# Performance work log

Hardware: AMD Instinct MI355X
Metric: run time of the kernel (lower is better)

The kernel has to match this reference:

```python
import jax, jax.numpy as jnp
import numpy as np

B, C, H, W = 32, 512, 32, 32


def setup_inputs() -> dict:
    key = jax.random.key(0)
    ks = jax.random.split(key, 7)
    c2 = C // 2
    s_in = (1.0 / C) ** 0.5   # torch Conv2d default init scale (kernel 1x1)
    s_c2 = (1.0 / c2) ** 0.5
    return {
        "x": jax.random.normal(ks[0], (B, C, H, W), jnp.float32),
        "Wk": jax.random.normal(ks[1], (c2, C), jnp.float32) * s_in,
        "bk": jax.random.normal(ks[2], (c2,), jnp.float32) * s_in,
        "Wv": jax.random.normal(ks[3], (c2, C), jnp.float32) * s_in,
        "bv": jax.random.normal(ks[4], (c2,), jnp.float32) * s_in,
        "Wo": jax.random.normal(ks[5], (C, c2), jnp.float32) * s_c2,
        "bo": jax.random.normal(ks[6], (C,), jnp.float32) * s_c2,
    }


def reference(x, Wk, bk, Wv, bv, Wo, bo):
    Bn, Cn, Hn, Wn = x.shape
    c2 = Cn // 2
    M = Hn * Wn
    # 1x1 convs as channel contractions
    k = jnp.einsum('oc,bchw->bohw', Wk, x) + bk[None, :, None, None]   # [B,c2,H,W]
    v = jnp.einsum('oc,bchw->bohw', Wv, x) + bv[None, :, None, None]   # [B,c2,H,W]
    # torch .reshape(B, M, c2) reinterprets memory (NOT a transpose) -> same in jnp
    v = v.reshape(Bn, M, c2)                                           # [B,M,c2]
    kf = k.reshape(Bn, c2, M)                                          # [B,c2,M]
    # cov_feature: k^T I_hat k with I_hat = (1/M)I - (1/M^2)11^T
    #            = (1/M) k^T k - (1/M^2) s s^T,  s = sum over channels
    gram = jnp.einsum('bcm,bcn->bmn', kf, kf) / M                      # [B,M,M]
    s = kf.sum(axis=1)                                                 # [B,M]
    cov = gram - (s[:, :, None] * s[:, None, :]) / (M * M)
    attn = jax.nn.softmax(cov * (c2 ** -0.5), axis=-1)                 # [B,M,M]
    out = jnp.einsum('bmn,bnc->bmc', attn, v)                          # [B,M,c2]
    # torch .view(B, c2, H, W) is also a raw memory reinterpretation
    out = out.reshape(Bn, c2, Hn, Wn)
    out = jnp.einsum('oc,bchw->bohw', Wo, out) + bo[None, :, None, None]
    return out + x
```

## Files before the change

### kernel.cpp

```cpp
#include <hip/hip_runtime.h>


typedef short bf8 __attribute__((ext_vector_type(8)));
typedef float f32x4 __attribute__((ext_vector_type(4)));

#define MFMA16(a, b, c) __builtin_amdgcn_mfma_f32_16x16x32_bf16((a), (b), (c), 0, 0, 0)

__device__ __forceinline__ short f2bf(float x) {
  unsigned u = __float_as_uint(x);
  u += 0x7fffu + ((u >> 16) & 1u);
  return (short)(u >> 16);
}

__device__ __forceinline__ void gll16(const short* g, void* l) {
  __builtin_amdgcn_global_load_lds(
      (const __attribute__((address_space(1))) unsigned int*)g,
      (__attribute__((address_space(3))) unsigned int*)l, 16, 0, 0);
}

__device__ __forceinline__ void gemm_core(const short* __restrict__ A,
                                          const short* __restrict__ B,
                                          int ldA, int ldB, int ksteps,
                                          char* smem, f32x4 acc[4][4]) {
  const int tid = threadIdx.x;
  const int w = tid >> 6, l = tid & 63;
  const int q = l >> 4, i = l & 15;
  const int wm = w & 1, wn = w >> 1;
  const int srow = l >> 3;
  const int gcol = ((l & 7) ^ srow) * 8;
  f32x4 zz = {0.f, 0.f, 0.f, 0.f};
  #pragma unroll
  for (int mt = 0; mt < 4; ++mt)
    #pragma unroll
    for (int nt = 0; nt < 4; ++nt) acc[mt][nt] = zz;

  for (int ks = 0; ks < ksteps; ++ks) {
    __syncthreads();
    const short* Ak = A + ks * 64 + gcol;
    const short* Bk = B + ks * 64 + gcol;
    #pragma unroll
    for (int j = 0; j < 4; ++j) {
      int s = w * 4 + j;
      size_t row = (size_t)(s * 8 + srow);
      gll16(Ak + row * ldA, smem + s * 1024);
      gll16(Bk + row * ldB, smem + 16384 + s * 1024);
    }
    __syncthreads();
    #pragma unroll
    for (int kq = 0; kq < 2; ++kq) {
      int sw = ((kq * 4 + q) ^ (i & 7)) * 16;
      bf8 af[4], bq[4];
      #pragma unroll
      for (int mt = 0; mt < 4; ++mt)
        af[mt] = *(const bf8*)(smem + (wm * 64 + mt * 16 + i) * 128 + sw);
      #pragma unroll
      for (int nt = 0; nt < 4; ++nt)
        bq[nt] = *(const bf8*)(smem + 16384 + (wn * 64 + nt * 16 + i) * 128 + sw);
      #pragma unroll
      for (int mt = 0; mt < 4; ++mt)
        #pragma unroll
        for (int nt = 0; nt < 4; ++nt)
          acc[mt][nt] = MFMA16(af[mt], bq[nt], acc[mt][nt]);
    }
  }
}

__global__ __launch_bounds__(256) void p0_xpose(const float* __restrict__ x,
                                                short* __restrict__ xT) {
  __shared__ float lds[64][65];
  int cb = blockIdx.x, sb = blockIdx.y, b = blockIdx.z;
  int t = threadIdx.x;
  int c0 = cb * 64, sp0 = sb * 64;
  const float4* x4 = reinterpret_cast<const float4*>(x);
  #pragma unroll
  for (int j = 0; j < 4; ++j) {
    int lin = t + 256 * j;
    int cl = lin >> 4, s4 = lin & 15;
    float4 v = x4[(((size_t)b * 512 + c0 + cl) * 1024 + sp0 + s4 * 4) >> 2];
    lds[cl][s4 * 4 + 0] = v.x; lds[cl][s4 * 4 + 1] = v.y;
    lds[cl][s4 * 4 + 2] = v.z; lds[cl][s4 * 4 + 3] = v.w;
  }
  __syncthreads();
  int spl = t >> 2, cs = (t & 3) * 16;
  bf8 o0, o1;
  #pragma unroll
  for (int j = 0; j < 8; ++j) o0[j] = f2bf(lds[cs + j][spl]);
  #pragma unroll
  for (int j = 0; j < 8; ++j) o1[j] = f2bf(lds[cs + 8 + j][spl]);
  size_t base = ((size_t)b * 1024 + sp0 + spl) * 512 + c0 + cs;
  *reinterpret_cast<bf8*>(xT + base) = o0;
  *reinterpret_cast<bf8*>(xT + base + 8) = o1;
}

__global__ __launch_bounds__(256) void w0_weights(const float* __restrict__ Wk,
                                                  const float* __restrict__ Wv,
                                                  const float* __restrict__ Wo,
                                                  short* __restrict__ Wkv_bf,
                                                  short* __restrict__ Wo_bf) {
  int g = blockIdx.x * 256 + threadIdx.x;
  if (g < 262144) {
    int o = g >> 9, c = g & 511;
    float v = (o < 256) ? Wk[o * 512 + c] : Wv[(o - 256) * 512 + c];
    Wkv_bf[g] = f2bf(v);
  } else {
    int i2 = g - 262144;
    Wo_bf[i2] = f2bf(Wo[i2]);
  }
}

__global__ __launch_bounds__(256, 2) void k1_kv(const short* __restrict__ xT,
                                                const short* __restrict__ Wkv,
                                                const float* __restrict__ bk,
                                                const float* __restrict__ bv,
                                                short* __restrict__ kT,
                                                short* __restrict__ vT,
                                                float* __restrict__ s_part) {
  __shared__ __attribute__((aligned(16))) char smem[32768];
  f32x4 acc[4][4];
  int bm = blockIdx.x, bn = blockIdx.y;
  gemm_core(xT + (size_t)bm * 128 * 512, Wkv + (size_t)bn * 128 * 512,
            512, 512, 8, smem, acc);
  int tid = threadIdx.x;
  int w = tid >> 6, l = tid & 63, q = l >> 4, i = l & 15;
  int wm = w & 1, wn = w >> 1;
  int mbase = bm * 128 + wm * 64;
  int nbase = bn * 128 + wn * 64;
  if (bn < 2) {
    float rp[4][4];
    #pragma unroll
    for (int mt = 0; mt < 4; ++mt)
      #pragma unroll
      for (int r = 0; r < 4; ++r) rp[mt][r] = 0.f;
    #pragma unroll
    for (int mt = 0; mt < 4; ++mt)
      #pragma unroll
      for (int nt = 0; nt < 4; ++nt) {
        float bias = bk[nbase + nt * 16 + i];
        #pragma unroll
        for (int r = 0; r < 4; ++r) {
          float val = acc[mt][nt][r] + bias;
          int mg = mbase + mt * 16 + q * 4 + r;
          kT[(size_t)mg * 256 + nbase + nt * 16 + i] = f2bf(val);
          rp[mt][r] += val;
        }
      }
    #pragma unroll
    for (int mask = 1; mask <= 8; mask <<= 1)
      #pragma unroll
      for (int mt = 0; mt < 4; ++mt)
        #pragma unroll
        for (int r = 0; r < 4; ++r) rp[mt][r] += __shfl_xor(rp[mt][r], mask, 64);
    if (i == 0) {
      int pg = bn * 2 + wn;
      #pragma unroll
      for (int mt = 0; mt < 4; ++mt)
        #pragma unroll
        for (int r = 0; r < 4; ++r)
          s_part[pg * 32768 + mbase + mt * 16 + q * 4 + r] = rp[mt][r];
    }
  } else {
    #pragma unroll
    for (int mt = 0; mt < 4; ++mt)
      #pragma unroll
      for (int nt = 0; nt < 4; ++nt) {
        int o2 = nbase + nt * 16 + i - 256;
        float bias = bv[o2];
        #pragma unroll
        for (int r = 0; r < 4; ++r) {
          float val = acc[mt][nt][r] + bias;
          int mg = mbase + mt * 16 + q * 4 + r;
          int b = mg >> 10, sp = mg & 1023;
          vT[((size_t)b * 256 + (sp & 255)) * 1024 + 4 * o2 + (sp >> 8)] = f2bf(val);
        }
      }
  }
}

__global__ __launch_bounds__(256) void k1b_sum(const float* __restrict__ s_part,
                                               float* __restrict__ s_buf) {
  int t = blockIdx.x * 256 + threadIdx.x;
  s_buf[t] = s_part[t] + s_part[32768 + t] + s_part[65536 + t] + s_part[98304 + t];
}

__global__ __launch_bounds__(256, 2) void k2_fused(const short* __restrict__ kT,
                                                   const short* __restrict__ vT,
                                                   const float* __restrict__ s_buf,
                                                   short* __restrict__ OB) {
  __shared__ __attribute__((aligned(16))) char smem[81920];
  char* Apan = smem;
  char* Ppan = smem + 32768;
  char* Bst  = smem + 49152;

  const int bm = blockIdx.x, b = blockIdx.y;
  const int tid = threadIdx.x;
  const int w = tid >> 6, l = tid & 63;
  const int q = l >> 4, i = l & 15;
  const int srow = l >> 3;
  const int gcol = ((l & 7) ^ srow) * 8;

  const short* kTb = kT + (size_t)b * 1024 * 256;
  const short* vTb = vT + (size_t)b * 256 * 1024;
  const float* sB = s_buf + b * 1024;

  {
    const short* Am = kTb + (size_t)bm * 64 * 256;
    #pragma unroll
    for (int ks = 0; ks < 4; ++ks)
      #pragma unroll
      for (int j2 = 0; j2 < 2; ++j2) {
        int s2 = w * 2 + j2;
        gll16(Am + (size_t)(s2 * 8 + srow) * 256 + ks * 64 + gcol,
              Apan + ks * 8192 + s2 * 1024);
      }
  }

  float sm[4][4];
  #pragma unroll
  for (int mt = 0; mt < 4; ++mt)
    #pragma unroll
    for (int r = 0; r < 4; ++r) sm[mt][r] = sB[bm * 64 + mt * 16 + q * 4 + r];

  f32x4 zz = {0.f, 0.f, 0.f, 0.f};
  f32x4 acc_o[4][4];
  #pragma unroll
  for (int mt = 0; mt < 4; ++mt)
    #pragma unroll
    for (int ct = 0; ct < 4; ++ct) acc_o[mt][ct] = zz;
  float rowsum[4][4];
  #pragma unroll
  for (int mt = 0; mt < 4; ++mt)
    #pragma unroll
    for (int r = 0; r < 4; ++r) rowsum[mt][r] = 0.f;

  const float sc1 = 1.0f / 16384.0f;
  const float sc2 = 1.0f / 16777216.0f;

  for (int n0 = 0; n0 < 1024; n0 += 128) {
    f32x4 acc_s[4][2];
    #pragma unroll
    for (int mt = 0; mt < 4; ++mt)
      #pragma unroll
      for (int nt = 0; nt < 2; ++nt) acc_s[mt][nt] = zz;
    const short* Bn = kTb + (size_t)n0 * 256;
    for (int ks = 0; ks < 4; ++ks) {
      __syncthreads();
      #pragma unroll
      for (int j = 0; j < 4; ++j) {
        int s = w * 4 + j;
        gll16(Bn + (size_t)(s * 8 + srow) * 256 + ks * 64 + gcol, Bst + s * 1024);
      }
      __syncthreads();
      #pragma unroll
      for (int kq = 0; kq < 2; ++kq) {
        int sw = ((kq * 4 + q) ^ (i & 7)) * 16;
        bf8 af[4], bq2[2];
        #pragma unroll
        for (int mt = 0; mt < 4; ++mt)
          af[mt] = *(const bf8*)(Apan + ks * 8192 + (mt * 16 + i) * 128 + sw);
        #pragma unroll
        for (int nt = 0; nt < 2; ++nt)
          bq2[nt] = *(const bf8*)(Bst + (w * 32 + nt * 16 + i) * 128 + sw);
        #pragma unroll
        for (int mt = 0; mt < 4; ++mt)
          #pragma unroll
          for (int nt = 0; nt < 2; ++nt)
            acc_s[mt][nt] = MFMA16(af[mt], bq2[nt], acc_s[mt][nt]);
      }
    }
    float sn0 = sB[n0 + w * 32 + i];
    float sn1 = sB[n0 + w * 32 + 16 + i];
    #pragma unroll
    for (int nt = 0; nt < 2; ++nt) {
      float sn = nt ? sn1 : sn0;
      int nl = w * 32 + nt * 16 + i;
      char* pbase = Ppan + (nl >> 6) * 8192 + (nl & 7) * 2;
      int gchunk = (nl >> 3) & 7;
      #pragma unroll
      for (int mt = 0; mt < 4; ++mt)
        #pragma unroll
        for (int r = 0; r < 4; ++r) {
          int ml = mt * 16 + q * 4 + r;
          float p = __expf(acc_s[mt][nt][r] * sc1 - sm[mt][r] * sn * sc2);
          rowsum[mt][r] += p;
          *(short*)(pbase + ml * 128 + ((gchunk ^ (ml & 7)) * 16)) = f2bf(p);
        }
    }
    for (int ks2 = 0; ks2 < 2; ++ks2) {
      __syncthreads();
      #pragma unroll
      for (int j = 0; j < 8; ++j) {
        int s = w * 8 + j;
        gll16(vTb + (size_t)(s * 8 + srow) * 1024 + n0 + ks2 * 64 + gcol,
              Bst + s * 1024);
      }
      __syncthreads();
      #pragma unroll
      for (int kq = 0; kq < 2; ++kq) {
        int sw = ((kq * 4 + q) ^ (i & 7)) * 16;
        bf8 ap[4], bv4[4];
        #pragma unroll
        for (int mt = 0; mt < 4; ++mt)
          ap[mt] = *(const bf8*)(Ppan + ks2 * 8192 + (mt * 16 + i) * 128 + sw);
        #pragma unroll
        for (int ct = 0; ct < 4; ++ct)
          bv4[ct] = *(const bf8*)(Bst + (w * 64 + ct * 16 + i) * 128 + sw);
        #pragma unroll
        for (int mt = 0; mt < 4; ++mt)
          #pragma unroll
          for (int ct = 0; ct < 4; ++ct)
            acc_o[mt][ct] = MFMA16(ap[mt], bv4[ct], acc_o[mt][ct]);
      }
    }
  }
  #pragma unroll
  for (int mask = 1; mask <= 8; mask <<= 1)
    #pragma unroll
    for (int mt = 0; mt < 4; ++mt)
      #pragma unroll
      for (int r = 0; r < 4; ++r) rowsum[mt][r] += __shfl_xor(rowsum[mt][r], mask, 64);
  __syncthreads();
  float* rs = (float*)Ppan;
  if (i == 0) {
    #pragma unroll
    for (int mt = 0; mt < 4; ++mt)
      #pragma unroll
      for (int r = 0; r < 4; ++r)
        rs[w * 64 + mt * 16 + q * 4 + r] = rowsum[mt][r];
  }
  __syncthreads();
  float rinv[4][4];
  #pragma unroll
  for (int mt = 0; mt < 4; ++mt)
    #pragma unroll
    for (int r = 0; r < 4; ++r) {
      int m = mt * 16 + q * 4 + r;
      rinv[mt][r] = 1.0f / (rs[m] + rs[64 + m] + rs[128 + m] + rs[192 + m]);
    }
  short* ob = (short*)(Bst + w * 8192);
  #pragma unroll
  for (int mt = 0; mt < 4; ++mt)
    #pragma unroll
    for (int ct = 0; ct < 4; ++ct)
      #pragma unroll
      for (int r = 0; r < 4; ++r)
        ob[(r * 64 + ct * 16 + i) * 16 + mt * 4 + q] =
            f2bf(acc_o[mt][ct][r] * rinv[mt][r]);
  short* obg = OB + (size_t)b * 1024 * 256;
  #pragma unroll
  for (int jj = 0; jj < 8; ++jj) {
    int lr = jj * 32 + (l >> 1), ch = l & 1;
    bf8 vv = *(const bf8*)(ob + lr * 16 + ch * 8);
    int rr = lr >> 6, cc = lr & 63;
    *(bf8*)(obg + ((size_t)(rr * 256 + w * 64 + cc)) * 256 + bm * 16 + ch * 8) = vv;
  }
}

__global__ __launch_bounds__(256, 2) void k3_out(const short* __restrict__ Wo_bf,
                                                 const short* __restrict__ OB,
                                                 const float* __restrict__ bo,
                                                 const float* __restrict__ x,
                                                 float* __restrict__ out) {
  __shared__ __attribute__((aligned(16))) char smem[32768];
  f32x4 acc[4][4];
  int bm = blockIdx.x, bn = blockIdx.y, b = blockIdx.z;
  gemm_core(Wo_bf + (size_t)bm * 128 * 256,
            OB + ((size_t)b * 1024 + bn * 128) * 256, 256, 256, 4, smem, acc);
  int tid = threadIdx.x;
  int w = tid >> 6, l = tid & 63, q = l >> 4, i = l & 15;
  int wm = w & 1, wn = w >> 1;
  int oloc = bm * 128 + wm * 64, sploc = bn * 128 + wn * 64;
  #pragma unroll
  for (int mt = 0; mt < 4; ++mt)
    #pragma unroll
    for (int r = 0; r < 4; ++r) {
      int o = oloc + mt * 16 + q * 4 + r;
      float bias = bo[o];
      #pragma unroll
      for (int nt = 0; nt < 4; ++nt) {
        int sp = sploc + nt * 16 + i;
        size_t idx = ((size_t)b * 512 + o) * 1024 + sp;
        out[idx] = acc[mt][nt][r] + bias + x[idx];
      }
    }
}

extern "C" void kernel_launch(void* const* d_in, const int* in_sizes, int n_in,
                              void* d_out, int out_size, void* d_ws, size_t ws_size,
                              hipStream_t stream) {
  (void)in_sizes; (void)n_in; (void)out_size; (void)ws_size;
  const float* x  = (const float*)d_in[0];
  const float* Wk = (const float*)d_in[1];
  const float* bk = (const float*)d_in[2];
  const float* Wv = (const float*)d_in[3];
  const float* bv = (const float*)d_in[4];
  const float* Wo = (const float*)d_in[5];
  const float* bo = (const float*)d_in[6];
  float* out = (float*)d_out;
  char* ws = (char*)d_ws;

  short* xT     = (short*)(ws);
  short* OB     = (short*)(ws);
  short* kTb    = (short*)(ws + 33554432);
  short* vTb    = (short*)(ws + 50331648);
  short* Wkv_bf = (short*)(ws + 67108864);
  short* Wo_bf  = (short*)(ws + 67633152);
  float* s_part = (float*)(ws + 67895296);
  float* s_buf  = (float*)(ws + 68419584);

  p0_xpose<<<dim3(8, 16, 32), 256, 0, stream>>>(x, xT);
  w0_weights<<<1536, 256, 0, stream>>>(Wk, Wv, Wo, Wkv_bf, Wo_bf);
  k1_kv<<<dim3(256, 4), 256, 0, stream>>>(xT, Wkv_bf, bk, bv, kTb, vTb, s_part);
  k1b_sum<<<128, 256, 0, stream>>>(s_part, s_buf);
  k2_fused<<<dim3(16, 32), 256, 0, stream>>>(kTb, vTb, s_buf, OB);
  k3_out<<<dim3(4, 8, 32), 256, 0, stream>>>(Wo_bf, OB, bo, x, out);
}
```

Baseline: 246.6 us.

## Double-buffer per-wave K/V slabs in fused attention kernel with relaxed barriers

Restructures the k2_fused main loop so each wave stages its own K and V slabs into two alternating LDS buffers, prefetching the next stage while computing the current one. Most block-wide __syncthreads are replaced by vmcnt/lgkmcnt waits and a relaxed barrier. The kernel also raises MFMA priority via s_setprio, precomputes the s-scaling terms, and remaps a 1D grid so that batches are grouped per XCD for L2 locality. The risk is subtle hazards from the hand-written waitcnt values and higher register pressure from full unrolling.

After: 233.0 us. -5.5%, faster.

```diff
diff --git a/kernel.cpp b/kernel.cpp
--- a/kernel.cpp
+++ b/kernel.cpp
@@ -16,6 +16,22 @@
   __builtin_amdgcn_global_load_lds(
       (const __attribute__((address_space(1))) unsigned int*)g,
       (__attribute__((address_space(3))) unsigned int*)l, 16, 0, 0);
+}
+
+__device__ __forceinline__ void lgkm0() {
+  asm volatile("s_waitcnt lgkmcnt(0)" ::: "memory");
+}
+template <int N>
+__device__ __forceinline__ void waitv() {
+  static_assert(N == 0 || N == 4 || N == 8, "bad vmcnt");
+  if constexpr (N == 0) asm volatile("s_waitcnt vmcnt(0)" ::: "memory");
+  else if constexpr (N == 4) asm volatile("s_waitcnt vmcnt(4)" ::: "memory");
+  else asm volatile("s_waitcnt vmcnt(8)" ::: "memory");
+}
+__device__ __forceinline__ void barrier_relaxed() {
+  asm volatile("" ::: "memory");
+  __builtin_amdgcn_s_barrier();
+  asm volatile("" ::: "memory");
 }
 
 __device__ __forceinline__ void gemm_core(const short* __restrict__ A,
@@ -191,7 +207,11 @@
   char* Ppan = smem + 32768;
   char* Bst  = smem + 49152;
 
-  const int bm = blockIdx.x, b = blockIdx.y;
+  const int id = blockIdx.x;
+  const int xcd = id & 7, slot = id >> 3;
+  const int b  = xcd * 4 + (slot >> 4);
+  const int bm = slot & 15;
+
   const int tid = threadIdx.x;
   const int w = tid >> 6, l = tid & 63;
   const int q = l >> 4, i = l & 15;
@@ -202,6 +222,38 @@
   const short* vTb = vT + (size_t)b * 256 * 1024;
   const float* sB = s_buf + b * 1024;
 
+  char* slabA = Bst + w * 4096;
+  char* slabB = Bst + 16384 + w * 4096;
+
+  const float sc1 = 1.0f / 16384.0f;
+  const float sc2 = 1.0f / 16777216.0f;
+
+  float sm2[4][4];
+  #pragma unroll
+  for (int mt = 0; mt < 4; ++mt)
+    #pragma unroll
+    for (int r = 0; r < 4; ++r)
+      sm2[mt][r] = sB[bm * 64 + mt * 16 + q * 4 + r] * sc2;
+  float sn[8][2];
+  #pragma unroll
+  for (int c = 0; c < 8; ++c) {
+    sn[c][0] = sB[c * 128 + w * 32 + i];
+    sn[c][1] = sB[c * 128 + w * 32 + 16 + i];
+  }
+
+  auto stageS = [&](int c, int ks, char* sl) {
+    const short* Bn = kTb + (size_t)c * 128 * 256 + ks * 64 + gcol;
+    #pragma unroll
+    for (int j = 0; j < 4; ++j)
+      gll16(Bn + (size_t)(w * 32 + j * 8 + srow) * 256, sl + j * 1024);
+  };
+  auto stageV = [&](int c, int ks2, int h, char* sl) {
+    const short* Vn = vTb + c * 128 + ks2 * 64 + gcol;
+    #pragma unroll
+    for (int j = 0; j < 4; ++j)
+      gll16(Vn + (size_t)(w * 64 + h * 32 + j * 8 + srow) * 1024, sl + j * 1024);
+  };
+
   {
     const short* Am = kTb + (size_t)bm * 64 * 256;
     #pragma unroll
@@ -213,43 +265,35 @@
               Apan + ks * 8192 + s2 * 1024);
       }
   }
-
-  float sm[4][4];
-  #pragma unroll
-  for (int mt = 0; mt < 4; ++mt)
-    #pragma unroll
-    for (int r = 0; r < 4; ++r) sm[mt][r] = sB[bm * 64 + mt * 16 + q * 4 + r];
+  stageS(0, 0, slabA);
+  stageS(0, 1, slabB);
+  waitv<8>();
+  barrier_relaxed();
 
   f32x4 zz = {0.f, 0.f, 0.f, 0.f};
   f32x4 acc_o[4][4];
+  float rowsum[4][4];
   #pragma unroll
   for (int mt = 0; mt < 4; ++mt)
     #pragma unroll
     for (int ct = 0; ct < 4; ++ct) acc_o[mt][ct] = zz;
-  float rowsum[4][4];
   #pragma unroll
   for (int mt = 0; mt < 4; ++mt)
     #pragma unroll
     for (int r = 0; r < 4; ++r) rowsum[mt][r] = 0.f;
 
-  const float sc1 = 1.0f / 16384.0f;
-  const float sc2 = 1.0f / 16777216.0f;
-
-  for (int n0 = 0; n0 < 1024; n0 += 128) {
+  #pragma unroll
+  for (int c = 0; c < 8; ++c) {
     f32x4 acc_s[4][2];
     #pragma unroll
     for (int mt = 0; mt < 4; ++mt)
       #pragma unroll
       for (int nt = 0; nt < 2; ++nt) acc_s[mt][nt] = zz;
-    const short* Bn = kTb + (size_t)n0 * 256;
+
+    #pragma unroll
     for (int ks = 0; ks < 4; ++ks) {
-      __syncthreads();
-      #pragma unroll
-      for (int j = 0; j < 4; ++j) {
-        int s = w * 4 + j;
-        gll16(Bn + (size_t)(s * 8 + srow) * 256 + ks * 64 + gcol, Bst + s * 1024);
-      }
-      __syncthreads();
+      char* sl = (ks & 1) ? slabB : slabA;
+      waitv<4>();
       #pragma unroll
       for (int kq = 0; kq < 2; ++kq) {
         int sw = ((kq * 4 + q) ^ (i & 7)) * 16;
@@ -259,19 +303,24 @@
           af[mt] = *(const bf8*)(Apan + ks * 8192 + (mt * 16 + i) * 128 + sw);
         #pragma unroll
         for (int nt = 0; nt < 2; ++nt)
-          bq2[nt] = *(const bf8*)(Bst + (w * 32 + nt * 16 + i) * 128 + sw);
+          bq2[nt] = *(const bf8*)(sl + (nt * 16 + i) * 128 + sw);
+        __builtin_amdgcn_s_setprio(1);
         #pragma unroll
         for (int mt = 0; mt < 4; ++mt)
           #pragma unroll
           for (int nt = 0; nt < 2; ++nt)
             acc_s[mt][nt] = MFMA16(af[mt], bq2[nt], acc_s[mt][nt]);
-      }
-    }
-    float sn0 = sB[n0 + w * 32 + i];
-    float sn1 = sB[n0 + w * 32 + 16 + i];
+        __builtin_amdgcn_s_setprio(0);
+      }
+      lgkm0();
+      if (ks < 2) stageS(c, ks + 2, sl);
+      else        stageV(c, 0, ks - 2, sl);
+    }
+
+    barrier_relaxed();
     #pragma unroll
     for (int nt = 0; nt < 2; ++nt) {
-      float sn = nt ? sn1 : sn0;
+      float snv = sn[c][nt];
       int nl = w * 32 + nt * 16 + i;
       char* pbase = Ppan + (nl >> 6) * 8192 + (nl & 7) * 2;
       int gchunk = (nl >> 3) & 7;
@@ -280,38 +329,43 @@
         #pragma unroll
         for (int r = 0; r < 4; ++r) {
           int ml = mt * 16 + q * 4 + r;
-          float p = __expf(acc_s[mt][nt][r] * sc1 - sm[mt][r] * sn * sc2);
+          float p = __expf(acc_s[mt][nt][r] * sc1 - sm2[mt][r] * snv);
           rowsum[mt][r] += p;
           *(short*)(pbase + ml * 128 + ((gchunk ^ (ml & 7)) * 16)) = f2bf(p);
         }
     }
-    for (int ks2 = 0; ks2 < 2; ++ks2) {
-      __syncthreads();
-      #pragma unroll
-      for (int j = 0; j < 8; ++j) {
-        int s = w * 8 + j;
-        gll16(vTb + (size_t)(s * 8 + srow) * 1024 + n0 + ks2 * 64 + gcol,
-              Bst + s * 1024);
-      }
-      __syncthreads();
+    lgkm0();
+    barrier_relaxed();
+
+    #pragma unroll
+    for (int pv = 0; pv < 4; ++pv) {
+      char* sl = (pv & 1) ? slabB : slabA;
+      const int ks2 = pv >> 1, h = pv & 1;
+      if (c == 7 && pv == 3) waitv<0>(); else waitv<4>();
       #pragma unroll
       for (int kq = 0; kq < 2; ++kq) {
         int sw = ((kq * 4 + q) ^ (i & 7)) * 16;
-        bf8 ap[4], bv4[4];
+        bf8 ap[4], bv2[2];
         #pragma unroll
         for (int mt = 0; mt < 4; ++mt)
           ap[mt] = *(const bf8*)(Ppan + ks2 * 8192 + (mt * 16 + i) * 128 + sw);
         #pragma unroll
-        for (int ct = 0; ct < 4; ++ct)
-          bv4[ct] = *(const bf8*)(Bst + (w * 64 + ct * 16 + i) * 128 + sw);
+        for (int u = 0; u < 2; ++u)
+          bv2[u] = *(const bf8*)(sl + (u * 16 + i) * 128 + sw);
+        __builtin_amdgcn_s_setprio(1);
         #pragma unroll
         for (int mt = 0; mt < 4; ++mt)
           #pragma unroll
-          for (int ct = 0; ct < 4; ++ct)
-            acc_o[mt][ct] = MFMA16(ap[mt], bv4[ct], acc_o[mt][ct]);
-      }
-    }
-  }
+          for (int u = 0; u < 2; ++u)
+            acc_o[mt][h * 2 + u] = MFMA16(ap[mt], bv2[u], acc_o[mt][h * 2 + u]);
+        __builtin_amdgcn_s_setprio(0);
+      }
+      lgkm0();
+      if (pv < 2) stageV(c, 1, pv, sl);
+      else if (c < 7) stageS(c + 1, pv - 2, sl);
+    }
+  }
+
   #pragma unroll
   for (int mask = 1; mask <= 8; mask <<= 1)
     #pragma unroll
@@ -411,6 +465,6 @@
   w0_weights<<<1536, 256, 0, stream>>>(Wk, Wv, Wo, Wkv_bf, Wo_bf);
   k1_kv<<<dim3(256, 4), 256, 0, stream>>>(xT, Wkv_bf, bk, bv, kTb, vTb, s_part);
   k1b_sum<<<128, 256, 0, stream>>>(s_part, s_buf);
-  k2_fused<<<dim3(16, 32), 256, 0, stream>>>(kTb, vTb, s_buf, OB);
+  k2_fused<<<dim3(512), 256, 0, stream>>>(kTb, vTb, s_buf, OB);
   k3_out<<<dim3(4, 8, 32), 256, 0, stream>>>(Wo_bf, OB, bo, x, out);
 }
```
